# Performance work log

Measured on AMD Instinct MI355X. Metric: run time of the kernel, lower is better.

The kernel has to match this reference:

```python
import jax, jax.numpy as jnp
import numpy as np

N_NODES = 100000
N_EDGES = 1600000
EMBED_DIM = 128
HIDDEN_DIM = 256


def setup_inputs() -> dict:
    key = jax.random.key(0)
    k_emb, k_src, k_dst, k_w1, k_w2 = jax.random.split(key, 5)
    emb = jax.random.normal(k_emb, (N_NODES, EMBED_DIM), dtype=jnp.float32)
    edge_src = jax.random.randint(k_src, (N_EDGES,), 0, N_NODES)
    edge_dst = jax.random.randint(k_dst, (N_EDGES,), 0, N_NODES)
    # Linear(2D -> H) and Linear(H -> D), stored as [in, out] for x @ W
    W1 = jax.random.normal(k_w1, (2 * EMBED_DIM, HIDDEN_DIM), dtype=jnp.float32) * (1.0 / np.sqrt(2 * EMBED_DIM))
    b1 = jnp.zeros((HIDDEN_DIM,), dtype=jnp.float32)
    W2 = jax.random.normal(k_w2, (HIDDEN_DIM, EMBED_DIM), dtype=jnp.float32) * (1.0 / np.sqrt(HIDDEN_DIM))
    b2 = jnp.zeros((EMBED_DIM,), dtype=jnp.float32)
    return {"emb": emb, "edge_src": edge_src, "edge_dst": edge_dst,
            "W1": W1, "b1": b1, "W2": W2, "b2": b2}


def reference(emb, edge_src, edge_dst, W1, b1, W2, b2):
    N, D = emb.shape
    E = edge_src.shape[0]
    # gather neighbor embeddings and segment-mean per destination node
    gathered = emb[edge_src]                                    # [E, D]
    nbr_sum = jax.ops.segment_sum(gathered, edge_dst, num_segments=N)   # [N, D]
    counts = jax.ops.segment_sum(jnp.ones((E,), emb.dtype), edge_dst, num_segments=N)  # [N]
    nbr_mean = nbr_sum / jnp.maximum(counts, 1.0)[:, None]
    # nodes with no neighbors fall back to their own embedding
    nbr_mean = jnp.where(counts[:, None] == 0, emb, nbr_mean)
    concat = jnp.concatenate([emb, nbr_mean], axis=-1)          # [N, 2D]
    h = jax.nn.relu(concat @ W1 + b1)                           # [N, H]
    return h @ W2 + b2                                          # [N, D]
```

## Files before the change

kernel.cpp:

```cpp
#include <hip/hip_runtime.h>

#define DD 128
#define HH 256
#define K1 256
#define BM 64
#define CH 2048
#define CH1 2048
#define CAP 4096

typedef __bf16 bf16;
typedef __attribute__((ext_vector_type(8))) __bf16 bf16x8;
typedef __attribute__((ext_vector_type(4))) float f32x4;
typedef __attribute__((ext_vector_type(2))) float f32x2;


__global__ __launch_bounds__(256) void countb_k(const int* __restrict__ dst,
                                                int* __restrict__ bcnt,
                                                int E, int BSH) {
    __shared__ int c[1024];
    for (int j = threadIdx.x; j < 1024; j += 256) c[j] = 0;
    __syncthreads();
    for (int e = blockIdx.x * 256 + threadIdx.x; e < E; e += gridDim.x * 256)
        atomicAdd(&c[dst[e] >> BSH], 1);
    __syncthreads();
    for (int j = threadIdx.x; j < 1024; j += 256)
        if (c[j]) atomicAdd(&bcnt[j], c[j]);
}

__global__ __launch_bounds__(1024) void scanb_k(const int* __restrict__ bcnt,
                                                int* __restrict__ bbase,
                                                int* __restrict__ bpos,
                                                int NB, int E) {
    __shared__ int s[1024];
    const int t = threadIdx.x;
    int v = (t < NB) ? bcnt[t] : 0;
    s[t] = v;
    __syncthreads();
    for (int off = 1; off < 1024; off <<= 1) {
        int y = (t >= off) ? s[t - off] : 0;
        __syncthreads();
        s[t] += y;
        __syncthreads();
    }
    int excl = s[t] - v;
    if (t < NB) { bbase[t] = excl; bpos[t] = excl; }
    if (t == 0) bbase[NB] = E;
}

__global__ __launch_bounds__(256) void part_k(const int* __restrict__ src,
                                              const int* __restrict__ dst,
                                              int* __restrict__ bpos,
                                              unsigned* __restrict__ pairs,
                                              int E, int BSH, int Bm1) {
    __shared__ int lcnt[1024];
    __shared__ int lbase[1024];
    const int t = threadIdx.x;
    const int e0 = blockIdx.x * CH1;
    const int e1 = min(E, e0 + CH1);
    for (int j = t; j < 1024; j += 256) lcnt[j] = 0;
    __syncthreads();
    int rs[CH1 / 256];
    #pragma unroll
    for (int k = 0; k < CH1 / 256; ++k) {
        int e = e0 + k * 256 + t;
        int b = -1;
        if (e < e1) { b = dst[e] >> BSH; atomicAdd(&lcnt[b], 1); }
        rs[k] = b;
    }
    __syncthreads();
    for (int j = t; j < 1024; j += 256) {
        int c = lcnt[j];
        lbase[j] = c ? atomicAdd(&bpos[j], c) : 0;
        lcnt[j] = 0;
    }
    __syncthreads();
    #pragma unroll
    for (int k = 0; k < CH1 / 256; ++k) {
        int e = e0 + k * 256 + t;
        if (e < e1) {
            int b = rs[k];
            int slot = lbase[b] + atomicAdd(&lcnt[b], 1);
            pairs[slot] = ((unsigned)(dst[e] & Bm1) << 24) | (unsigned)src[e];
        }
    }
}

__global__ __launch_bounds__(256) void sortb_k(const unsigned* __restrict__ pairs,
                                               const int* __restrict__ bbase,
                                               int* __restrict__ offs,
                                               int* __restrict__ ssrc,
                                               int N, int BSH) {
    __shared__ int hist[256];
    __shared__ int pref[256];
    __shared__ int run[256];
    __shared__ int sorted[CAP];
    const int t = threadIdx.x;
    const int b = blockIdx.x;
    const int B = 1 << BSH;
    const int d0 = b << BSH;
    const int nd = min(B, N - d0);
    const int rb = bbase[b], re = bbase[b + 1];
    const int cntE = re - rb;
    hist[t] = 0;
    __syncthreads();
    for (int i = rb + t; i < re; i += 256)
        atomicAdd(&hist[pairs[i] >> 24], 1);
    __syncthreads();
    pref[t] = hist[t];
    __syncthreads();
    for (int off = 1; off < 256; off <<= 1) {
        int y = (t >= off) ? pref[t - off] : 0;
        __syncthreads();
        pref[t] += y;
        __syncthreads();
    }
    if (t < nd) offs[d0 + t] = rb + pref[t];
    run[t] = pref[t] - hist[t];
    __syncthreads();
    if (cntE <= CAP) {
        for (int i = rb + t; i < re; i += 256) {
            unsigned p = pairs[i];
            int pos = atomicAdd(&run[p >> 24], 1);
            sorted[pos] = (int)(p & 0xFFFFFFu);
        }
        __syncthreads();
        for (int i = t; i < cntE; i += 256) ssrc[rb + i] = sorted[i];
    } else {
        for (int i = rb + t; i < re; i += 256) {
            unsigned p = pairs[i];
            int pos = atomicAdd(&run[p >> 24], 1);
            ssrc[rb + pos] = (int)(p & 0xFFFFFFu);
        }
    }
}


__global__ __launch_bounds__(256) void hist_k(const int* __restrict__ dst,
                                              int* __restrict__ cnt, int E) {
    for (int e = blockIdx.x * blockDim.x + threadIdx.x; e < E;
         e += gridDim.x * blockDim.x)
        atomicAdd(&cnt[dst[e]], 1);
}

__global__ __launch_bounds__(256) void scan1_k(const int* __restrict__ cnt,
                                               int* __restrict__ offs,
                                               int* __restrict__ part, int N) {
    __shared__ int sdata[256];
    const int b = blockIdx.x, t = threadIdx.x;
    const int base = b * 1024 + t * 4;
    int v[4], sum = 0;
    #pragma unroll
    for (int i = 0; i < 4; ++i) {
        int idx = base + i;
        v[i] = (idx < N) ? cnt[idx] : 0;
        sum += v[i];
    }
    sdata[t] = sum;
    __syncthreads();
    for (int off = 1; off < 256; off <<= 1) {
        int y = (t >= off) ? sdata[t - off] : 0;
        __syncthreads();
        sdata[t] += y;
        __syncthreads();
    }
    int excl = sdata[t] - sum;
    if (t == 255) part[b] = sdata[255];
    int run = excl;
    #pragma unroll
    for (int i = 0; i < 4; ++i) {
        int idx = base + i;
        if (idx < N) offs[idx] = run;
        run += v[i];
    }
}

__global__ __launch_bounds__(128) void scan2_k(int* __restrict__ part, int nparts) {
    __shared__ int sdata[128];
    const int t = threadIdx.x;
    int v = (t < nparts) ? part[t] : 0;
    sdata[t] = v;
    __syncthreads();
    for (int off = 1; off < 128; off <<= 1) {
        int y = (t >= off) ? sdata[t - off] : 0;
        __syncthreads();
        sdata[t] += y;
        __syncthreads();
    }
    if (t < nparts) part[t] = sdata[t] - v;
}

__global__ __launch_bounds__(256) void scan3_k(int* __restrict__ offs,
                                               const int* __restrict__ part, int N) {
    for (int i = blockIdx.x * blockDim.x + threadIdx.x; i < N;
         i += gridDim.x * blockDim.x)
        offs[i] += part[i >> 10];
}

__global__ __launch_bounds__(256) void bucket_k(const int* __restrict__ src,
                                                const int* __restrict__ dst,
                                                int* __restrict__ offs,
                                                int* __restrict__ ssrc,
                                                int E, int N) {
    const int r = blockIdx.x & 7;
    const int chunk = blockIdx.x >> 3;
    const int lo = r * (N >> 3);
    const int hi = (r == 7) ? N : lo + (N >> 3);
    const int e0 = chunk * CH;
    const int e1 = min(E, e0 + CH);
    for (int e = e0 + threadIdx.x; e < e1; e += 256) {
        int d = dst[e];
        if (d >= lo && d < hi) {
            int pos = atomicAdd(&offs[d], 1);
            ssrc[pos] = src[e];
        }
    }
}

__global__ __launch_bounds__(256) void gather_k(const float* __restrict__ emb,
                                                const int* __restrict__ offs,
                                                const int* __restrict__ ssrc,
                                                float* __restrict__ nbr, int N) {
    const int wid = threadIdx.x >> 6;
    const int lane = threadIdx.x & 63;
    const int d = blockIdx.x * 4 + wid;
    if (d >= N) return;
    const int sub = lane >> 5;
    const int c = (lane & 31) * 4;
    const int start = (d == 0) ? 0 : offs[d - 1];
    const int end = offs[d];
    float4 acc = make_float4(0.f, 0.f, 0.f, 0.f);
    int e = start;
    for (; e + 4 <= end; e += 4) {
        int s0 = ssrc[e + sub];
        int s1 = ssrc[e + 2 + sub];
        float4 v0 = *reinterpret_cast<const float4*>(&emb[(size_t)s0 * DD + c]);
        float4 v1 = *reinterpret_cast<const float4*>(&emb[(size_t)s1 * DD + c]);
        acc.x += v0.x + v1.x; acc.y += v0.y + v1.y;
        acc.z += v0.z + v1.z; acc.w += v0.w + v1.w;
    }
    for (; e + 2 <= end; e += 2) {
        int s = ssrc[e + sub];
        float4 v = *reinterpret_cast<const float4*>(&emb[(size_t)s * DD + c]);
        acc.x += v.x; acc.y += v.y; acc.z += v.z; acc.w += v.w;
    }
    if (e < end && sub == 0) {
        int s = ssrc[e];
        float4 v = *reinterpret_cast<const float4*>(&emb[(size_t)s * DD + c]);
        acc.x += v.x; acc.y += v.y; acc.z += v.z; acc.w += v.w;
    }
    acc.x += __shfl_xor(acc.x, 32);
    acc.y += __shfl_xor(acc.y, 32);
    acc.z += __shfl_xor(acc.z, 32);
    acc.w += __shfl_xor(acc.w, 32);
    if (sub == 0) {
        if (end > start) {
            float inv = 1.f / (float)(end - start);
            acc.x *= inv; acc.y *= inv; acc.z *= inv; acc.w *= inv;
        } else {
            acc = *reinterpret_cast<const float4*>(&emb[(size_t)d * DD + c]);
        }
        *reinterpret_cast<float4*>(&nbr[(size_t)d * DD + c]) = acc;
    }
}

__global__ __launch_bounds__(256) void cvt8_k(const float* __restrict__ emb,
                                              unsigned* __restrict__ emb8,
                                              size_t n8) {
    for (size_t i = blockIdx.x * blockDim.x + threadIdx.x; i < n8;
         i += (size_t)gridDim.x * blockDim.x) {
        float4 a = *reinterpret_cast<const float4*>(&emb[i * 8]);
        float4 b = *reinterpret_cast<const float4*>(&emb[i * 8 + 4]);
        int w0 = __builtin_amdgcn_cvt_pk_fp8_f32(a.x, a.y, 0, false);
        w0 = __builtin_amdgcn_cvt_pk_fp8_f32(a.z, a.w, w0, true);
        int w1 = __builtin_amdgcn_cvt_pk_fp8_f32(b.x, b.y, 0, false);
        w1 = __builtin_amdgcn_cvt_pk_fp8_f32(b.z, b.w, w1, true);
        uint2 o; o.x = (unsigned)w0; o.y = (unsigned)w1;
        *reinterpret_cast<uint2*>(&emb8[i * 2]) = o;
    }
}

__global__ __launch_bounds__(256) void gather8_k(const unsigned* __restrict__ emb8,
                                                 const float* __restrict__ emb,
                                                 const int* __restrict__ offs,
                                                 const int* __restrict__ ssrc,
                                                 bf16* __restrict__ nbrh, int N) {
    const int wid = threadIdx.x >> 6;
    const int lane = threadIdx.x & 63;
    const int d = blockIdx.x * 4 + wid;
    if (d >= N) return;
    const int slot = lane >> 4;
    const int c8 = (lane & 15) * 8;
    const int start = (d == 0) ? 0 : offs[d - 1];
    const int end = offs[d];
    float acc[8];
    #pragma unroll
    for (int j = 0; j < 8; ++j) acc[j] = 0.f;
    int e = start;
    for (; e + 8 <= end; e += 8) {
        int s0 = ssrc[e + slot];
        int s1 = ssrc[e + 4 + slot];
        uint2 v0 = *reinterpret_cast<const uint2*>(&emb8[((size_t)s0 * DD + c8) >> 2]);
        uint2 v1 = *reinterpret_cast<const uint2*>(&emb8[((size_t)s1 * DD + c8) >> 2]);
        f32x2 p;
        p = __builtin_amdgcn_cvt_pk_f32_fp8(v0.x, false); acc[0] += p[0]; acc[1] += p[1];
        p = __builtin_amdgcn_cvt_pk_f32_fp8(v0.x, true);  acc[2] += p[0]; acc[3] += p[1];
        p = __builtin_amdgcn_cvt_pk_f32_fp8(v0.y, false); acc[4] += p[0]; acc[5] += p[1];
        p = __builtin_amdgcn_cvt_pk_f32_fp8(v0.y, true);  acc[6] += p[0]; acc[7] += p[1];
        p = __builtin_amdgcn_cvt_pk_f32_fp8(v1.x, false); acc[0] += p[0]; acc[1] += p[1];
        p = __builtin_amdgcn_cvt_pk_f32_fp8(v1.x, true);  acc[2] += p[0]; acc[3] += p[1];
        p = __builtin_amdgcn_cvt_pk_f32_fp8(v1.y, false); acc[4] += p[0]; acc[5] += p[1];
        p = __builtin_amdgcn_cvt_pk_f32_fp8(v1.y, true);  acc[6] += p[0]; acc[7] += p[1];
    }
    for (; e + 4 <= end; e += 4) {
        int s0 = ssrc[e + slot];
        uint2 v0 = *reinterpret_cast<const uint2*>(&emb8[((size_t)s0 * DD + c8) >> 2]);
        f32x2 p;
        p = __builtin_amdgcn_cvt_pk_f32_fp8(v0.x, false); acc[0] += p[0]; acc[1] += p[1];
        p = __builtin_amdgcn_cvt_pk_f32_fp8(v0.x, true);  acc[2] += p[0]; acc[3] += p[1];
        p = __builtin_amdgcn_cvt_pk_f32_fp8(v0.y, false); acc[4] += p[0]; acc[5] += p[1];
        p = __builtin_amdgcn_cvt_pk_f32_fp8(v0.y, true);  acc[6] += p[0]; acc[7] += p[1];
    }
    if (slot < end - e) {
        int s0 = ssrc[e + slot];
        uint2 v0 = *reinterpret_cast<const uint2*>(&emb8[((size_t)s0 * DD + c8) >> 2]);
        f32x2 p;
        p = __builtin_amdgcn_cvt_pk_f32_fp8(v0.x, false); acc[0] += p[0]; acc[1] += p[1];
        p = __builtin_amdgcn_cvt_pk_f32_fp8(v0.x, true);  acc[2] += p[0]; acc[3] += p[1];
        p = __builtin_amdgcn_cvt_pk_f32_fp8(v0.y, false); acc[4] += p[0]; acc[5] += p[1];
        p = __builtin_amdgcn_cvt_pk_f32_fp8(v0.y, true);  acc[6] += p[0]; acc[7] += p[1];
    }
    #pragma unroll
    for (int j = 0; j < 8; ++j) {
        acc[j] += __shfl_xor(acc[j], 16);
        acc[j] += __shfl_xor(acc[j], 32);
    }
    if (slot == 0) {
        bf16x8 o;
        if (end > start) {
            float inv = 1.f / (float)(end - start);
            #pragma unroll
            for (int j = 0; j < 8; ++j) o[j] = (bf16)(acc[j] * inv);
        } else {
            float4 a = *reinterpret_cast<const float4*>(&emb[(size_t)d * DD + c8]);
            float4 b = *reinterpret_cast<const float4*>(&emb[(size_t)d * DD + c8 + 4]);
            o[0]=(bf16)a.x; o[1]=(bf16)a.y; o[2]=(bf16)a.z; o[3]=(bf16)a.w;
            o[4]=(bf16)b.x; o[5]=(bf16)b.y; o[6]=(bf16)b.z; o[7]=(bf16)b.w;
        }
        *reinterpret_cast<bf16x8*>(&nbrh[(size_t)d * DD + c8]) = o;
    }
}

__global__ __launch_bounds__(64) void packW_k(const float* __restrict__ W1,
                                              const float* __restrict__ W2,
                                              bf16* __restrict__ w1h,
                                              bf16* __restrict__ w2h) {
    const int bid = blockIdx.x;
    const float* W; bf16* outp; int NC; int rel;
    if (bid < 128) { W = W1; outp = w1h; NC = HH; rel = bid; }
    else           { W = W2; outp = w2h; NC = DD; rel = bid - 128; }
    const int ntiles = NC >> 4;
    const int kt = rel / ntiles;
    const int nt = rel % ntiles;
    const int l = threadIdx.x;
    const int k0 = kt * 32 + (l >> 4) * 8;
    const int n = nt * 16 + (l & 15);
    bf16x8 hv;
    #pragma unroll
    for (int r = 0; r < 8; ++r)
        hv[r] = (bf16)W[(size_t)(k0 + r) * NC + n];
    *reinterpret_cast<bf16x8*>(outp + ((size_t)rel * 64 + l) * 8) = hv;
}

__global__ __launch_bounds__(512) void mlp_mfma_k(const float* __restrict__ emb,
        const float* nbrf, const bf16* __restrict__ nbrh,
        const bf16* __restrict__ w1h, const float* __restrict__ b1,
        const bf16* __restrict__ w2h, const float* __restrict__ b2,
        float* out, int N) {
    __shared__ char smem[BM * K1 * 2];
    const int t = threadIdx.x;
    const int n0 = blockIdx.x * BM;
    const int l = t & 63;
    const int w = t >> 6;

    #pragma unroll
    for (int i = 0; i < 4; ++i) {
        int chunk = i * 512 + t;
        int row = chunk >> 5;
        int c0 = (chunk & 31) * 8;
        int n = n0 + row;
        bf16x8 hv;
        if (n < N) {
            if (c0 >= DD && nbrh != nullptr) {
                hv = *reinterpret_cast<const bf16x8*>(&nbrh[(size_t)n * DD + (c0 - DD)]);
            } else {
                const float* sp = (c0 < DD) ? &emb[(size_t)n * DD + c0]
                                            : &nbrf[(size_t)n * DD + (c0 - DD)];
                float4 a = *reinterpret_cast<const float4*>(sp);
                float4 b = *reinterpret_cast<const float4*>(sp + 4);
                hv[0]=(bf16)a.x; hv[1]=(bf16)a.y; hv[2]=(bf16)a.z; hv[3]=(bf16)a.w;
                hv[4]=(bf16)b.x; hv[5]=(bf16)b.y; hv[6]=(bf16)b.z; hv[7]=(bf16)b.w;
            }
        } else {
            #pragma unroll
            for (int j = 0; j < 8; ++j) hv[j] = (bf16)0.f;
        }
        int off = row * 512 + ((c0 * 2) ^ ((row & 7) << 4));
        *reinterpret_cast<bf16x8*>(smem + off) = hv;
    }
    __syncthreads();

    const int arow = l & 15;
    const int abyte = (l >> 4) * 16;

    f32x4 acc[4][2];
    #pragma unroll
    for (int ntl = 0; ntl < 2; ++ntl) {
        float bv = b1[w * 32 + ntl * 16 + (l & 15)];
        #pragma unroll
        for (int mt = 0; mt < 4; ++mt)
            acc[mt][ntl] = (f32x4){bv, bv, bv, bv};
    }
    for (int kt = 0; kt < 8; ++kt) {
        bf16x8 ah[4];
        #pragma unroll
        for (int mt = 0; mt < 4; ++mt) {
            int row = mt * 16 + arow;
            int off = row * 512 + ((kt * 64 + abyte) ^ ((row & 7) << 4));
            ah[mt] = *reinterpret_cast<const bf16x8*>(smem + off);
        }
        #pragma unroll
        for (int ntl = 0; ntl < 2; ++ntl) {
            int nt = w * 2 + ntl;
            size_t boff = ((size_t)(kt * 16 + nt) * 64 + l) * 8;
            bf16x8 bh = *reinterpret_cast<const bf16x8*>(w1h + boff);
            #pragma unroll
            for (int mt = 0; mt < 4; ++mt)
                acc[mt][ntl] = __builtin_amdgcn_mfma_f32_16x16x32_bf16(ah[mt], bh, acc[mt][ntl], 0, 0, 0);
        }
    }
    __syncthreads();

    #pragma unroll
    for (int mt = 0; mt < 4; ++mt)
        #pragma unroll
        for (int ntl = 0; ntl < 2; ++ntl) {
            int col = w * 32 + ntl * 16 + (l & 15);
            #pragma unroll
            for (int r = 0; r < 4; ++r) {
                int row = mt * 16 + (l >> 4) * 4 + r;
                int off = row * 512 + ((col * 2) ^ ((row & 7) << 4));
                *reinterpret_cast<bf16*>(smem + off) = (bf16)fmaxf(acc[mt][ntl][r], 0.f);
            }
        }
    __syncthreads();

    f32x4 acc2[4];
    {
        float bv = b2[w * 16 + (l & 15)];
        #pragma unroll
        for (int mt = 0; mt < 4; ++mt)
            acc2[mt] = (f32x4){bv, bv, bv, bv};
    }
    for (int kt = 0; kt < 8; ++kt) {
        bf16x8 ah[4];
        #pragma unroll
        for (int mt = 0; mt < 4; ++mt) {
            int row = mt * 16 + arow;
            int off = row * 512 + ((kt * 64 + abyte) ^ ((row & 7) << 4));
            ah[mt] = *reinterpret_cast<const bf16x8*>(smem + off);
        }
        size_t boff = ((size_t)(kt * 8 + w) * 64 + l) * 8;
        bf16x8 bh = *reinterpret_cast<const bf16x8*>(w2h + boff);
        #pragma unroll
        for (int mt = 0; mt < 4; ++mt)
            acc2[mt] = __builtin_amdgcn_mfma_f32_16x16x32_bf16(ah[mt], bh, acc2[mt], 0, 0, 0);
    }
    #pragma unroll
    for (int mt = 0; mt < 4; ++mt) {
        int col = w * 16 + (l & 15);
        #pragma unroll
        for (int r = 0; r < 4; ++r) {
            int row = mt * 16 + (l >> 4) * 4 + r;
            int n = n0 + row;
            if (n < N) out[(size_t)n * DD + col] = acc2[mt][r];
        }
    }
}

__global__ __launch_bounds__(256) void scatter_k(const float* __restrict__ emb,
        const int* __restrict__ src, const int* __restrict__ dst,
        float* nbr, float* __restrict__ cnt, int E) {
    int e = blockIdx.x * 8 + (threadIdx.x >> 5);
    if (e >= E) return;
    int lane = threadIdx.x & 31;
    int s = src[e];
    int d = dst[e];
    const float4 v = *reinterpret_cast<const float4*>(&emb[(size_t)s * DD + lane * 4]);
    float* o = &nbr[(size_t)d * DD + lane * 4];
    atomicAdd(o + 0, v.x);
    atomicAdd(o + 1, v.y);
    atomicAdd(o + 2, v.z);
    atomicAdd(o + 3, v.w);
    if (lane == 0) atomicAdd(&cnt[d], 1.0f);
}

__global__ __launch_bounds__(256) void mlp_k(const float* __restrict__ emb,
        const float* nbr, const float* cnt,
        const float* __restrict__ W1, const float* __restrict__ b1,
        const float* __restrict__ W2, const float* __restrict__ b2,
        float* out, int N) {
    __shared__ float smem[BM * K1];
    const int t = threadIdx.x;
    const int n0 = blockIdx.x * BM;
    #pragma unroll
    for (int it = 0; it < 16; ++it) {
        int idx = it * 256 + t;
        int r = idx >> 6;
        int c4 = idx & 63;
        int n = n0 + r;
        float4 v = make_float4(0.f, 0.f, 0.f, 0.f);
        if (n < N) {
            if (c4 < 32) {
                v = *reinterpret_cast<const float4*>(&emb[(size_t)n * DD + c4 * 4]);
            } else {
                float c = cnt[n];
                if (c > 0.f) {
                    v = *reinterpret_cast<const float4*>(&nbr[(size_t)n * DD + (c4 - 32) * 4]);
                    float inv = 1.f / c;
                    v.x *= inv; v.y *= inv; v.z *= inv; v.w *= inv;
                } else {
                    v = *reinterpret_cast<const float4*>(&emb[(size_t)n * DD + (c4 - 32) * 4]);
                }
            }
        }
        *reinterpret_cast<float4*>(&smem[idx * 4]) = v;
    }
    __syncthreads();
    const int tx = t & 31;
    const int ty = t >> 5;
    const int r0 = ty * 8;
    {
        const int c0 = tx * 8;
        float acc[8][8];
        const float4 bva = *reinterpret_cast<const float4*>(&b1[c0]);
        const float4 bvb = *reinterpret_cast<const float4*>(&b1[c0 + 4]);
        #pragma unroll
        for (int i = 0; i < 8; ++i) {
            acc[i][0] = bva.x; acc[i][1] = bva.y; acc[i][2] = bva.z; acc[i][3] = bva.w;
            acc[i][4] = bvb.x; acc[i][5] = bvb.y; acc[i][6] = bvb.z; acc[i][7] = bvb.w;
        }
        for (int k0 = 0; k0 < K1; k0 += 4) {
            float xs[8][4];
            #pragma unroll
            for (int i = 0; i < 8; ++i) {
                float4 xv = *reinterpret_cast<const float4*>(&smem[(r0 + i) * K1 + k0]);
                xs[i][0] = xv.x; xs[i][1] = xv.y; xs[i][2] = xv.z; xs[i][3] = xv.w;
            }
            #pragma unroll
            for (int kk = 0; kk < 4; ++kk) {
                const float4 wa = *reinterpret_cast<const float4*>(&W1[(size_t)(k0 + kk) * HH + c0]);
                const float4 wb = *reinterpret_cast<const float4*>(&W1[(size_t)(k0 + kk) * HH + c0 + 4]);
                #pragma unroll
                for (int i = 0; i < 8; ++i) {
                    float x = xs[i][kk];
                    acc[i][0] += x * wa.x; acc[i][1] += x * wa.y;
                    acc[i][2] += x * wa.z; acc[i][3] += x * wa.w;
                    acc[i][4] += x * wb.x; acc[i][5] += x * wb.y;
                    acc[i][6] += x * wb.z; acc[i][7] += x * wb.w;
                }
            }
        }
        __syncthreads();
        #pragma unroll
        for (int i = 0; i < 8; ++i) {
            float4 h0, h1;
            h0.x = fmaxf(acc[i][0], 0.f); h0.y = fmaxf(acc[i][1], 0.f);
            h0.z = fmaxf(acc[i][2], 0.f); h0.w = fmaxf(acc[i][3], 0.f);
            h1.x = fmaxf(acc[i][4], 0.f); h1.y = fmaxf(acc[i][5], 0.f);
            h1.z = fmaxf(acc[i][6], 0.f); h1.w = fmaxf(acc[i][7], 0.f);
            *reinterpret_cast<float4*>(&smem[(r0 + i) * HH + c0]) = h0;
            *reinterpret_cast<float4*>(&smem[(r0 + i) * HH + c0 + 4]) = h1;
        }
        __syncthreads();
    }
    {
        const int c0 = tx * 4;
        float acc[8][4];
        const float4 bv = *reinterpret_cast<const float4*>(&b2[c0]);
        #pragma unroll
        for (int i = 0; i < 8; ++i) {
            acc[i][0] = bv.x; acc[i][1] = bv.y; acc[i][2] = bv.z; acc[i][3] = bv.w;
        }
        for (int k0 = 0; k0 < HH; k0 += 4) {
            float hs[8][4];
            #pragma unroll
            for (int i = 0; i < 8; ++i) {
                float4 hv = *reinterpret_cast<const float4*>(&smem[(r0 + i) * HH + k0]);
                hs[i][0] = hv.x; hs[i][1] = hv.y; hs[i][2] = hv.z; hs[i][3] = hv.w;
            }
            #pragma unroll
            for (int kk = 0; kk < 4; ++kk) {
                const float4 w2 = *reinterpret_cast<const float4*>(&W2[(size_t)(k0 + kk) * DD + c0]);
                #pragma unroll
                for (int i = 0; i < 8; ++i) {
                    float h = hs[i][kk];
                    acc[i][0] += h * w2.x; acc[i][1] += h * w2.y;
                    acc[i][2] += h * w2.z; acc[i][3] += h * w2.w;
                }
            }
        }
        #pragma unroll
        for (int i = 0; i < 8; ++i) {
            int n = n0 + r0 + i;
            if (n < N) {
                float4 o;
                o.x = acc[i][0]; o.y = acc[i][1]; o.z = acc[i][2]; o.w = acc[i][3];
                *reinterpret_cast<float4*>(&out[(size_t)n * DD + c0]) = o;
            }
        }
    }
}

extern "C" void kernel_launch(void* const* d_in, const int* in_sizes, int n_in,
                              void* d_out, int out_size, void* d_ws, size_t ws_size,
                              hipStream_t stream) {
    const float* emb = (const float*)d_in[0];
    const int* esrc  = (const int*)d_in[1];
    const int* edst  = (const int*)d_in[2];
    const float* W1  = (const float*)d_in[3];
    const float* b1  = (const float*)d_in[4];
    const float* W2  = (const float*)d_in[5];
    const float* b2  = (const float*)d_in[6];
    float* out = (float*)d_out;

    const int N = in_sizes[0] / DD;
    const int E = in_sizes[1];
    const int nparts = (N + 1023) / 1024;

    int BSH = 0;
    while ((((size_t)N + ((size_t)1 << BSH) - 1) >> BSH) > 1024) ++BSH;
    const int B = 1 << BSH;
    const int NB = (N + B - 1) >> BSH;

    int* cnt  = (int*)d_ws;
    int* offs = cnt + N;
    int* part = offs + N;
    int* aux  = part + 128;
    int* ssrc = aux + 4096;
    char* wp = (char*)(ssrc + E);
    wp = (char*)(((uintptr_t)wp + 15) & ~(uintptr_t)15);
    bf16* w1h = (bf16*)wp;
    bf16* w2h = w1h + 65536;
    unsigned* emb8 = (unsigned*)(w2h + 32768);
    bf16* nbrh = (bf16*)(emb8 + (size_t)N * DD / 4);
    unsigned* pairs = emb8;
    int* bcnt  = aux;
    int* bbase = aux + 1024;
    int* bpos  = aux + 2560;
    const size_t need_base = (size_t)((char*)(w2h + 32768) - (char*)d_ws);
    const size_t need_full = (size_t)((char*)(nbrh + (size_t)N * DD) - (char*)d_ws);
    const bool pairs_fit = ((size_t)E * 4 <= (size_t)N * DD / 4 * 4 + (size_t)N * DD * 2);

    if (ws_size >= need_base && nparts <= 128) {
        const bool fast = (ws_size >= need_full) && pairs_fit && (BSH <= 8) &&
                          (N < (1 << 24)) && ((N & 7) == 0) && (NB <= 1024);
        packW_k<<<dim3(192), dim3(64), 0, stream>>>(W1, W2, w1h, w2h);
        if (fast) {
            hipMemsetAsync(bcnt, 0, 1024 * sizeof(int), stream);
            countb_k<<<dim3(512), dim3(256), 0, stream>>>(edst, bcnt, E, BSH);
            scanb_k<<<dim3(1), dim3(1024), 0, stream>>>(bcnt, bbase, bpos, NB, E);
            part_k<<<dim3((E + CH1 - 1) / CH1), dim3(256), 0, stream>>>(
                esrc, edst, bpos, pairs, E, BSH, B - 1);
            sortb_k<<<dim3(NB), dim3(256), 0, stream>>>(pairs, bbase, offs, ssrc, N, BSH);
            cvt8_k<<<dim3(2048), dim3(256), 0, stream>>>(emb, emb8, (size_t)N * DD / 8);
            gather8_k<<<dim3((N + 3) / 4), dim3(256), 0, stream>>>(emb8, emb, offs, ssrc, nbrh, N);
            mlp_mfma_k<<<dim3((N + BM - 1) / BM), dim3(512), 0, stream>>>(
                emb, nullptr, nbrh, w1h, b1, w2h, b2, out, N);
        } else {
            hipMemsetAsync(cnt, 0, (size_t)N * sizeof(int), stream);
            hist_k<<<dim3(1024), dim3(256), 0, stream>>>(edst, cnt, E);
            scan1_k<<<dim3(nparts), dim3(256), 0, stream>>>(cnt, offs, part, N);
            scan2_k<<<dim3(1), dim3(128), 0, stream>>>(part, nparts);
            scan3_k<<<dim3(512), dim3(256), 0, stream>>>(offs, part, N);
            const int nchunks = (E + CH - 1) / CH;
            bucket_k<<<dim3(nchunks * 8), dim3(256), 0, stream>>>(esrc, edst, offs, ssrc, E, N);
            gather_k<<<dim3((N + 3) / 4), dim3(256), 0, stream>>>(emb, offs, ssrc, out, N);
            mlp_mfma_k<<<dim3((N + BM - 1) / BM), dim3(512), 0, stream>>>(
                emb, out, nullptr, w1h, b1, w2h, b2, out, N);
        }
    } else {
        float* fcnt = (float*)d_ws;
        hipMemsetAsync(out, 0, (size_t)N * DD * sizeof(float), stream);
        hipMemsetAsync(fcnt, 0, (size_t)N * sizeof(float), stream);
        scatter_k<<<dim3((E + 7) / 8), dim3(256), 0, stream>>>(emb, esrc, edst, out, fcnt, E);
        mlp_k<<<dim3((N + BM - 1) / BM), dim3(256), 0, stream>>>(
            emb, out, fcnt, W1, b1, W2, b2, out, N);
    }
}
```

Measured before the change: 169.8 us.

## Stage partition output in LDS with fewer, larger buckets and unroll gather

```diff
diff --git a/kernel.cpp b/kernel.cpp
--- a/kernel.cpp
+++ b/kernel.cpp
@@ -5,8 +5,8 @@
 #define K1 256
 #define BM 64
 #define CH 2048
-#define CH1 2048
-#define CAP 4096
+#define CHP 8192
+#define CAP 8192
 
 typedef __bf16 bf16;
 typedef __attribute__((ext_vector_type(8))) __bf16 bf16x8;
@@ -17,26 +17,26 @@
 __global__ __launch_bounds__(256) void countb_k(const int* __restrict__ dst,
                                                 int* __restrict__ bcnt,
                                                 int E, int BSH) {
-    __shared__ int c[1024];
-    for (int j = threadIdx.x; j < 1024; j += 256) c[j] = 0;
+    __shared__ int c[512];
+    for (int j = threadIdx.x; j < 512; j += 256) c[j] = 0;
     __syncthreads();
     for (int e = blockIdx.x * 256 + threadIdx.x; e < E; e += gridDim.x * 256)
         atomicAdd(&c[dst[e] >> BSH], 1);
     __syncthreads();
-    for (int j = threadIdx.x; j < 1024; j += 256)
+    for (int j = threadIdx.x; j < 512; j += 256)
         if (c[j]) atomicAdd(&bcnt[j], c[j]);
 }
 
-__global__ __launch_bounds__(1024) void scanb_k(const int* __restrict__ bcnt,
-                                                int* __restrict__ bbase,
-                                                int* __restrict__ bpos,
-                                                int NB, int E) {
-    __shared__ int s[1024];
+__global__ __launch_bounds__(512) void scanb_k(const int* __restrict__ bcnt,
+                                               int* __restrict__ bbase,
+                                               int* __restrict__ bpos,
+                                               int NB, int E) {
+    __shared__ int s[512];
     const int t = threadIdx.x;
     int v = (t < NB) ? bcnt[t] : 0;
     s[t] = v;
     __syncthreads();
-    for (int off = 1; off < 1024; off <<= 1) {
+    for (int off = 1; off < 512; off <<= 1) {
         int y = (t >= off) ? s[t - off] : 0;
         __syncthreads();
         s[t] += y;
@@ -52,36 +52,50 @@
                                               int* __restrict__ bpos,
                                               unsigned* __restrict__ pairs,
                                               int E, int BSH, int Bm1) {
-    __shared__ int lcnt[1024];
-    __shared__ int lbase[1024];
+    __shared__ int lcnt[512];
+    __shared__ int lpref[512];
+    __shared__ int lrun[512];
+    __shared__ int gbase[512];
+    __shared__ unsigned stage[CHP];
     const int t = threadIdx.x;
-    const int e0 = blockIdx.x * CH1;
-    const int e1 = min(E, e0 + CH1);
-    for (int j = t; j < 1024; j += 256) lcnt[j] = 0;
-    __syncthreads();
-    int rs[CH1 / 256];
-    #pragma unroll
-    for (int k = 0; k < CH1 / 256; ++k) {
-        int e = e0 + k * 256 + t;
-        int b = -1;
-        if (e < e1) { b = dst[e] >> BSH; atomicAdd(&lcnt[b], 1); }
-        rs[k] = b;
-    }
-    __syncthreads();
-    for (int j = t; j < 1024; j += 256) {
+    const int e0 = blockIdx.x * CHP;
+    const int e1 = min(E, e0 + CHP);
+    for (int j = t; j < 512; j += 256) lcnt[j] = 0;
+    __syncthreads();
+    for (int e = e0 + t; e < e1; e += 256)
+        atomicAdd(&lcnt[dst[e] >> BSH], 1);
+    __syncthreads();
+    for (int j = t; j < 512; j += 256) lpref[j] = lcnt[j];
+    __syncthreads();
+    for (int off = 1; off < 512; off <<= 1) {
+        int j2 = t + 256;
+        int v0 = (t >= off) ? lpref[t - off] : 0;
+        int v1 = (j2 >= off) ? lpref[j2 - off] : 0;
+        __syncthreads();
+        lpref[t] += v0;
+        lpref[j2] += v1;
+        __syncthreads();
+    }
+    for (int j = t; j < 512; j += 256) {
         int c = lcnt[j];
-        lbase[j] = c ? atomicAdd(&bpos[j], c) : 0;
-        lcnt[j] = 0;
-    }
-    __syncthreads();
-    #pragma unroll
-    for (int k = 0; k < CH1 / 256; ++k) {
-        int e = e0 + k * 256 + t;
-        if (e < e1) {
-            int b = rs[k];
-            int slot = lbase[b] + atomicAdd(&lcnt[b], 1);
-            pairs[slot] = ((unsigned)(dst[e] & Bm1) << 24) | (unsigned)src[e];
-        }
+        gbase[j] = c ? atomicAdd(&bpos[j], c) : 0;
+        lrun[j] = lpref[j] - c;
+    }
+    __syncthreads();
+    for (int e = e0 + t; e < e1; e += 256) {
+        int d = dst[e];
+        int b = d >> BSH;
+        int pos = atomicAdd(&lrun[b], 1);
+        stage[pos] = ((unsigned)(d & Bm1) << 24) | (unsigned)src[e];
+    }
+    __syncthreads();
+    const int wv = t >> 6, ln = t & 63;
+    for (int b = wv; b < 512; b += 4) {
+        int s = lpref[b] - lcnt[b];
+        int c = lcnt[b];
+        int g = gbase[b];
+        for (int i = ln; i < c; i += 64)
+            pairs[g + i] = stage[s + i];
     }
 }
 
@@ -90,9 +104,9 @@
                                                int* __restrict__ offs,
                                                int* __restrict__ ssrc,
                                                int N, int BSH) {
-    __shared__ int hist[256];
-    __shared__ int pref[256];
-    __shared__ int run[256];
+    __shared__ int hist[512];
+    __shared__ int pref[512];
+    __shared__ int run[512];
     __shared__ int sorted[CAP];
     const int t = threadIdx.x;
     const int b = blockIdx.x;
@@ -101,21 +115,24 @@
     const int nd = min(B, N - d0);
     const int rb = bbase[b], re = bbase[b + 1];
     const int cntE = re - rb;
-    hist[t] = 0;
+    for (int j = t; j < 512; j += 256) hist[j] = 0;
     __syncthreads();
     for (int i = rb + t; i < re; i += 256)
         atomicAdd(&hist[pairs[i] >> 24], 1);
     __syncthreads();
-    pref[t] = hist[t];
-    __syncthreads();
-    for (int off = 1; off < 256; off <<= 1) {
-        int y = (t >= off) ? pref[t - off] : 0;
-        __syncthreads();
-        pref[t] += y;
-        __syncthreads();
-    }
-    if (t < nd) offs[d0 + t] = rb + pref[t];
-    run[t] = pref[t] - hist[t];
+    for (int j = t; j < 512; j += 256) pref[j] = hist[j];
+    __syncthreads();
+    for (int off = 1; off < 512; off <<= 1) {
+        int j2 = t + 256;
+        int v0 = (t >= off) ? pref[t - off] : 0;
+        int v1 = (j2 >= off) ? pref[j2 - off] : 0;
+        __syncthreads();
+        pref[t] += v0;
+        pref[j2] += v1;
+        __syncthreads();
+    }
+    for (int j = t; j < nd; j += 256) offs[d0 + j] = rb + pref[j];
+    for (int j = t; j < 512; j += 256) run[j] = pref[j] - hist[j];
     __syncthreads();
     if (cntE <= CAP) {
         for (int i = rb + t; i < re; i += 256) {
@@ -279,6 +296,14 @@
     }
 }
 
+__device__ __forceinline__ void acc8(float* acc, uint2 v) {
+    f32x2 p;
+    p = __builtin_amdgcn_cvt_pk_f32_fp8(v.x, false); acc[0] += p[0]; acc[1] += p[1];
+    p = __builtin_amdgcn_cvt_pk_f32_fp8(v.x, true);  acc[2] += p[0]; acc[3] += p[1];
+    p = __builtin_amdgcn_cvt_pk_f32_fp8(v.y, false); acc[4] += p[0]; acc[5] += p[1];
+    p = __builtin_amdgcn_cvt_pk_f32_fp8(v.y, true);  acc[6] += p[0]; acc[7] += p[1];
+}
+
 __global__ __launch_bounds__(256) void gather8_k(const unsigned* __restrict__ emb8,
                                                  const float* __restrict__ emb,
                                                  const int* __restrict__ offs,
@@ -296,38 +321,33 @@
     #pragma unroll
     for (int j = 0; j < 8; ++j) acc[j] = 0.f;
     int e = start;
+    for (; e + 16 <= end; e += 16) {
+        int s0 = ssrc[e + slot];
+        int s1 = ssrc[e + 4 + slot];
+        int s2 = ssrc[e + 8 + slot];
+        int s3 = ssrc[e + 12 + slot];
+        uint2 v0 = *reinterpret_cast<const uint2*>(&emb8[((size_t)s0 * DD + c8) >> 2]);
+        uint2 v1 = *reinterpret_cast<const uint2*>(&emb8[((size_t)s1 * DD + c8) >> 2]);
+        uint2 v2 = *reinterpret_cast<const uint2*>(&emb8[((size_t)s2 * DD + c8) >> 2]);
+        uint2 v3 = *reinterpret_cast<const uint2*>(&emb8[((size_t)s3 * DD + c8) >> 2]);
+        acc8(acc, v0); acc8(acc, v1); acc8(acc, v2); acc8(acc, v3);
+    }
     for (; e + 8 <= end; e += 8) {
         int s0 = ssrc[e + slot];
         int s1 = ssrc[e + 4 + slot];
         uint2 v0 = *reinterpret_cast<const uint2*>(&emb8[((size_t)s0 * DD + c8) >> 2]);
         uint2 v1 = *reinterpret_cast<const uint2*>(&emb8[((size_t)s1 * DD + c8) >> 2]);
-        f32x2 p;
-        p = __builtin_amdgcn_cvt_pk_f32_fp8(v0.x, false); acc[0] += p[0]; acc[1] += p[1];
-        p = __builtin_amdgcn_cvt_pk_f32_fp8(v0.x, true);  acc[2] += p[0]; acc[3] += p[1];
-        p = __builtin_amdgcn_cvt_pk_f32_fp8(v0.y, false); acc[4] += p[0]; acc[5] += p[1];
-        p = __builtin_amdgcn_cvt_pk_f32_fp8(v0.y, true);  acc[6] += p[0]; acc[7] += p[1];
-        p = __builtin_amdgcn_cvt_pk_f32_fp8(v1.x, false); acc[0] += p[0]; acc[1] += p[1];
-        p = __builtin_amdgcn_cvt_pk_f32_fp8(v1.x, true);  acc[2] += p[0]; acc[3] += p[1];
-        p = __builtin_amdgcn_cvt_pk_f32_fp8(v1.y, false); acc[4] += p[0]; acc[5] += p[1];
-        p = __builtin_amdgcn_cvt_pk_f32_fp8(v1.y, true);  acc[6] += p[0]; acc[7] += p[1];
+        acc8(acc, v0); acc8(acc, v1);
     }
     for (; e + 4 <= end; e += 4) {
         int s0 = ssrc[e + slot];
         uint2 v0 = *reinterpret_cast<const uint2*>(&emb8[((size_t)s0 * DD + c8) >> 2]);
-        f32x2 p;
-        p = __builtin_amdgcn_cvt_pk_f32_fp8(v0.x, false); acc[0] += p[0]; acc[1] += p[1];
-        p = __builtin_amdgcn_cvt_pk_f32_fp8(v0.x, true);  acc[2] += p[0]; acc[3] += p[1];
-        p = __builtin_amdgcn_cvt_pk_f32_fp8(v0.y, false); acc[4] += p[0]; acc[5] += p[1];
-        p = __builtin_amdgcn_cvt_pk_f32_fp8(v0.y, true);  acc[6] += p[0]; acc[7] += p[1];
+        acc8(acc, v0);
     }
     if (slot < end - e) {
         int s0 = ssrc[e + slot];
         uint2 v0 = *reinterpret_cast<const uint2*>(&emb8[((size_t)s0 * DD + c8) >> 2]);
-        f32x2 p;
-        p = __builtin_amdgcn_cvt_pk_f32_fp8(v0.x, false); acc[0] += p[0]; acc[1] += p[1];
-        p = __builtin_amdgcn_cvt_pk_f32_fp8(v0.x, true);  acc[2] += p[0]; acc[3] += p[1];
-        p = __builtin_amdgcn_cvt_pk_f32_fp8(v0.y, false); acc[4] += p[0]; acc[5] += p[1];
-        p = __builtin_amdgcn_cvt_pk_f32_fp8(v0.y, true);  acc[6] += p[0]; acc[7] += p[1];
+        acc8(acc, v0);
     }
     #pragma unroll
     for (int j = 0; j < 8; ++j) {
@@ -638,7 +658,7 @@
     const int nparts = (N + 1023) / 1024;
 
     int BSH = 0;
-    while ((((size_t)N + ((size_t)1 << BSH) - 1) >> BSH) > 1024) ++BSH;
+    while ((((size_t)N + ((size_t)1 << BSH) - 1) >> BSH) > 512) ++BSH;
     const int B = 1 << BSH;
     const int NB = (N + B - 1) >> BSH;
 
@@ -646,7 +666,7 @@
     int* offs = cnt + N;
     int* part = offs + N;
     int* aux  = part + 128;
-    int* ssrc = aux + 4096;
+    int* ssrc = aux + 2048;
     char* wp = (char*)(ssrc + E);
     wp = (char*)(((uintptr_t)wp + 15) & ~(uintptr_t)15);
     bf16* w1h = (bf16*)wp;
@@ -655,21 +675,21 @@
     bf16* nbrh = (bf16*)(emb8 + (size_t)N * DD / 4);
     unsigned* pairs = emb8;
     int* bcnt  = aux;
-    int* bbase = aux + 1024;
-    int* bpos  = aux + 2560;
+    int* bbase = aux + 512;
+    int* bpos  = aux + 1280;
     const size_t need_base = (size_t)((char*)(w2h + 32768) - (char*)d_ws);
     const size_t need_full = (size_t)((char*)(nbrh + (size_t)N * DD) - (char*)d_ws);
-    const bool pairs_fit = ((size_t)E * 4 <= (size_t)N * DD / 4 * 4 + (size_t)N * DD * 2);
+    const bool pairs_fit = ((size_t)E * 4 <= (size_t)N * DD);
 
     if (ws_size >= need_base && nparts <= 128) {
         const bool fast = (ws_size >= need_full) && pairs_fit && (BSH <= 8) &&
-                          (N < (1 << 24)) && ((N & 7) == 0) && (NB <= 1024);
+                          (N < (1 << 24)) && ((N & 7) == 0) && (NB <= 512);
         packW_k<<<dim3(192), dim3(64), 0, stream>>>(W1, W2, w1h, w2h);
         if (fast) {
-            hipMemsetAsync(bcnt, 0, 1024 * sizeof(int), stream);
+            hipMemsetAsync(bcnt, 0, 512 * sizeof(int), stream);
             countb_k<<<dim3(512), dim3(256), 0, stream>>>(edst, bcnt, E, BSH);
-            scanb_k<<<dim3(1), dim3(1024), 0, stream>>>(bcnt, bbase, bpos, NB, E);
-            part_k<<<dim3((E + CH1 - 1) / CH1), dim3(256), 0, stream>>>(
+            scanb_k<<<dim3(1), dim3(512), 0, stream>>>(bcnt, bbase, bpos, NB, E);
+            part_k<<<dim3((E + CHP - 1) / CHP), dim3(256), 0, stream>>>(
                 esrc, edst, bpos, pairs, E, BSH, B - 1);
             sortb_k<<<dim3(NB), dim3(256), 0, stream>>>(pairs, bbase, offs, ssrc, N, BSH);
             cvt8_k<<<dim3(2048), dim3(256), 0, stream>>>(emb, emb8, (size_t)N * DD / 8);
```

After: 177.4 us. 4.5% more time.
